# Kernel tuning notes

Hardware: AMD Instinct MI355X
Metric: run time of the kernel (lower is better)

Reference implementation:

```python
import jax, jax.numpy as jnp
import numpy as np
from jax import lax

B, L, D = 256, 512, 64
P, H, M, HOR, J = 256, 512, 256, 9, 12
EPS = 1e-5


def lstm_layer(xs, Wih, Whh, bih, bhh):
    """torch nn.LSTM single layer. xs: (B, L, Din). gates order i,f,g,o."""
    b, hdim = xs.shape[0], Whh.shape[1]
    WihT, WhhT = Wih.T, Whh.T
    bias = bih + bhh
    # precompute input contributions for all steps: (L, B, 4H)
    x_gates = jnp.swapaxes(xs @ WihT + bias, 0, 1)

    def step(carry, xg):
        h, c = carry
        gates = xg + h @ WhhT
        i, f, g, o = jnp.split(gates, 4, axis=-1)
        i = jax.nn.sigmoid(i)
        f = jax.nn.sigmoid(f)
        g = jnp.tanh(g)
        o = jax.nn.sigmoid(o)
        c = f * c + i * g
        h = o * jnp.tanh(c)
        return (h, c), h

    h0 = jnp.zeros((b, hdim), xs.dtype)
    c0 = jnp.zeros((b, hdim), xs.dtype)
    (_, _), hs = lax.scan(step, (h0, c0), x_gates)
    return jnp.swapaxes(hs, 0, 1)  # (B, L, H)


def setup_inputs() -> dict:
    key = jax.random.key(0)
    ks = jax.random.split(key, 16)
    g = lambda k, shape: (jax.random.normal(k, shape) * 0.05).astype(jnp.float32)
    z = lambda shape: jnp.zeros(shape, jnp.float32)
    return {
        "x": jax.random.normal(ks[0], (B, L, D), dtype=jnp.float32),
        "joint_index": jax.random.randint(ks[1], (B,), 0, J),
        "Wp": g(ks[2], (D, P)), "bp": z((P,)),
        "gamma": jnp.ones((P,), jnp.float32), "beta": z((P,)),
        "Wih0": g(ks[3], (4 * H, P)), "Whh0": g(ks[4], (4 * H, H)),
        "bih0": z((4 * H,)), "bhh0": z((4 * H,)),
        "Wih1": g(ks[5], (4 * H, H)), "Whh1": g(ks[6], (4 * H, H)),
        "bih1": z((4 * H,)), "bhh1": z((4 * H,)),
        "Wh1": g(ks[7], (J, H, M)), "bh1": z((J, M)),
        "Wh2": g(ks[8], (J, M, HOR)), "bh2": z((J, HOR)),
    }


def reference(x, joint_index, Wp, bp, gamma, beta,
              Wih0, Whh0, bih0, bhh0, Wih1, Whh1, bih1, bhh1,
              Wh1, bh1, Wh2, bh2):
    # input_proj: Linear -> LayerNorm -> GELU (exact erf form, torch default)
    h = x @ Wp + bp
    mu = h.mean(-1, keepdims=True)
    var = ((h - mu) ** 2).mean(-1, keepdims=True)
    h = gamma * (h - mu) * lax.rsqrt(var + EPS) + beta
    h = jax.nn.gelu(h, approximate=False)
    # 2-layer LSTM (dropout inactive at inference)
    h = lstm_layer(h, Wih0, Whh0, bih0, bhh0)
    h = lstm_layer(h, Wih1, Whh1, bih1, bhh1)
    h_last = h[:, -1, :]  # (B, H)
    # all 12 joint heads, then top-1 gather (matches torch stack+gather)
    z = jax.nn.gelu(jnp.einsum('bh,jhm->bjm', h_last, Wh1) + bh1, approximate=False)
    preds = jnp.einsum('bjm,jmo->bjo', z, Wh2) + bh2  # (B, J, HOR)
    return preds[jnp.arange(preds.shape[0]), joint_index]  # (B, HOR)
```

## Files before the change

kernel.cpp:

```cpp
#include <hip/hip_runtime.h>
#include <math.h>

typedef __bf16 bf16;
typedef __attribute__((ext_vector_type(8))) __bf16 bf16x8;
typedef __attribute__((ext_vector_type(4))) float f32x4;
typedef __attribute__((ext_vector_type(4))) int i32x4;

extern "C" __device__ i32x4 llvm_amdgcn_raw_buffer_load_v4i32(
    i32x4 rsrc, int voffset, int soffset, int cpol) __asm("llvm.amdgcn.raw.buffer.load.v4i32");

static constexpr int B = 256, L = 512, D = 64, P = 256, H = 512, M = 256, HOR = 9;
static constexpr int G = 2048;
static constexpr int K0 = P + H;
static constexpr int K1 = 2 * H;
static constexpr float EPS = 1e-5f;
static constexpr int NB = 6;
static constexpr int LDS_BYTES = 163840;

#define MFMA(a, b, c) __builtin_amdgcn_mfma_f32_16x16x32_bf16((a), (b), (c), 0, 0, 0)

__device__ __forceinline__ float sigmoidf_(float x) { return 1.0f / (1.0f + expf(-x)); }
__device__ __forceinline__ float gelu_exact(float x) {
    return 0.5f * x * (1.0f + erff(x * 0.70710678118654752f));
}

__device__ __forceinline__ void lds_barrier() {
    asm volatile("s_waitcnt lgkmcnt(0)" ::: "memory");
    __builtin_amdgcn_sched_barrier(0);
    __builtin_amdgcn_s_barrier();
    __builtin_amdgcn_sched_barrier(0);
}

__device__ __forceinline__ bf16x8 cload(const bf16* p) {
    union { unsigned long long u[2]; bf16x8 v; } r;
    const unsigned long long* q = (const unsigned long long*)p;
    r.u[0] = __hip_atomic_load(q,     __ATOMIC_RELAXED, __HIP_MEMORY_SCOPE_AGENT);
    r.u[1] = __hip_atomic_load(q + 1, __ATOMIC_RELAXED, __HIP_MEMORY_SCOPE_AGENT);
    return r.v;
}

__device__ __forceinline__ i32x4 make_rsrc(const void* p, unsigned bytes) {
    union { const void* p; unsigned u[2]; } a; a.p = p;
    i32x4 r;
    r.x = (int)a.u[0];
    r.y = (int)(a.u[1] & 0xFFFFu);
    r.z = (int)bytes;
    r.w = 0x00020000;
    return r;
}
__device__ __forceinline__ bf16x8 bload_sc0(i32x4 rsrc, int voff) {
    union { i32x4 i; bf16x8 b; } u;
    u.i = llvm_amdgcn_raw_buffer_load_v4i32(rsrc, voff, 0, 1 );
    return u.b;
}

__global__ __launch_bounds__(256) void emb_kernel(
    const float* __restrict__ x, const float* __restrict__ Wp,
    const float* __restrict__ bp, const float* __restrict__ gamma,
    const float* __restrict__ beta, bf16* __restrict__ ehi,
    bf16* __restrict__ elo, int use_elo)
{
    const int row = blockIdx.x;
    const int b   = row >> 9;
    const int t   = row & (L - 1);
    const int p   = threadIdx.x;
    __shared__ float xs[D];
    __shared__ float red[P];

    if (p < D) xs[p] = x[(size_t)row * D + p];
    __syncthreads();

    float acc = bp[p];
#pragma unroll
    for (int k = 0; k < D; ++k) acc = fmaf(xs[k], Wp[k * P + p], acc);

    red[p] = acc;
    __syncthreads();
    for (int s = 128; s > 0; s >>= 1) { if (p < s) red[p] += red[p + s]; __syncthreads(); }
    const float mu = red[0] * (1.0f / (float)P);
    __syncthreads();
    const float d = acc - mu;
    red[p] = d * d;
    __syncthreads();
    for (int s = 128; s > 0; s >>= 1) { if (p < s) red[p] += red[p + s]; __syncthreads(); }
    const float var = red[0] * (1.0f / (float)P);

    const float v = gelu_exact(gamma[p] * d * rsqrtf(var + EPS) + beta[p]);
    const size_t o = ((size_t)t * B + b) * P + p;
    const bf16 hh = (bf16)v;
    ehi[o] = hh;
    if (use_elo) elo[o] = (bf16)(v - (float)hh);
}

__global__ __launch_bounds__(64) void prep_w_frag(
    const float* __restrict__ Wih, const float* __restrict__ Whh, int Kih,
    bf16* __restrict__ hi, bf16* __restrict__ lo)
{
    const int ng = blockIdx.x, S = blockIdx.y, wc = blockIdx.z;
    const int lane = threadIdx.x;
    const int g = wc * 512 + ng * 16 + (lane & 15);
    const int kbase = S * 32 + (lane >> 4) * 8;
    const size_t out = ((((size_t)ng * gridDim.y + S) * 4 + wc) * 64 + lane) * 8;
#pragma unroll
    for (int e = 0; e < 8; ++e) {
        const int k = kbase + e;
        const float v = (k < Kih) ? Wih[(size_t)g * Kih + k]
                                  : Whh[(size_t)g * 512 + (k - Kih)];
        const bf16 h = (bf16)v;
        hi[out + e] = h;
        lo[out + e] = (bf16)(v - (float)h);
    }
}

__global__ __launch_bounds__(256) void prep_bias(
    const float* __restrict__ bih0, const float* __restrict__ bhh0,
    const float* __restrict__ bih1, const float* __restrict__ bhh1,
    float* __restrict__ bsum0, float* __restrict__ bsum1)
{
    const int g = blockIdx.x * 256 + threadIdx.x;
    bsum0[g] = bih0[g] + bhh0[g];
    bsum1[g] = bih1[g] + bhh1[g];
}

struct RArgs {
    int use_elo;
    const bf16 *ehi, *elo;
    const bf16 *W0hif, *W0lof, *W1hif, *W1lof;
    const float *bsum0, *bsum1;
    bf16 *h0hi[2], *h0lo[2], *h1hi[2], *h1lo[2];
    unsigned int* bar;
};

template <int NC, int LAYER>
__device__ __forceinline__ void tick_body(
    int tid, int lane, int wr2, int wc,
    int grow, int kin, int slot,
    const bf16* __restrict__ a0h, const bf16* __restrict__ a0l,
    i32x4 r1h, i32x4 r1l,
    char* lds, const bf16x8* wlo_own,
    float bI0, float bI1, float bF0, float bF1,
    float bG0, float bG1, float bO0, float bO1,
    float& c0r, float& c1r,
    unsigned int* hw_hi, unsigned int* hw_lo,
    int m, int jp)
{
    constexpr int K0seg = (LAYER == 0) ? 256 : 512;
    constexpr int AS0   = (LAYER == 0) ? 256 : 512;

    const bf16* wlds = (const bf16*)lds;
    char* dbuf = lds + 131072;
    float (*Gs)[68] = (float(*)[68])(lds + 131072);

    auto cloadA = [&](int c, int hf) -> bf16x8 {
        const int kk = c * 64 + kin;
        if (kk < K0seg) {
            const bf16* p = (hf ? a0l : a0h) + (size_t)grow * AS0 + kk;
            if (LAYER == 0) return *(const bf16x8*)p;
            return cload(p);
        }
        return bload_sc0(hf ? r1l : r1h, ((grow << 9) + (kk - K0seg)) * 2);
    };
    auto stageW = [&](const bf16x8& v, int pb, int hf) {
        *(bf16x8*)(dbuf + pb * 16384 + hf * 8192 + slot * 16) = v;
    };

    f32x4 hh[2], lh[2], hl[2];
#pragma unroll
    for (int i = 0; i < 2; ++i) {
        hh[i] = f32x4{0.f,0.f,0.f,0.f};
        lh[i] = f32x4{0.f,0.f,0.f,0.f};
        hl[i] = f32x4{0.f,0.f,0.f,0.f};
    }

    bf16x8 aregH[NB], aregL[NB];
#pragma unroll
    for (int i = 0; i < NB; ++i) { aregH[i] = cloadA(i, 0); aregL[i] = cloadA(i, 1); }
    stageW(aregH[0], 0, 0);
    stageW(aregL[0], 0, 1);
    aregH[0] = cloadA(NB, 0);
    aregL[0] = cloadA(NB, 1);
    lds_barrier();

#pragma unroll
    for (int c = 0; c < NC; ++c) {
        if (c + 1 < NC) {
            stageW(aregH[(c + 1) % NB], (c + 1) & 1, 0);
            stageW(aregL[(c + 1) % NB], (c + 1) & 1, 1);
            if (c + 1 + NB < NC) {
                aregH[(c + 1) % NB] = cloadA(c + 1 + NB, 0);
                aregL[(c + 1) % NB] = cloadA(c + 1 + NB, 1);
            }
        }
        const char* bufc = dbuf + (c & 1) * 16384;
#pragma unroll
        for (int s2 = 0; s2 < 2; ++s2) {
            const int S = c * 2 + s2;
            const int swz = ((s2 * 4) + (lane >> 4)) << 4;
            bf16x8 Whi = *(const bf16x8*)((const char*)wlds + ((S * 4 + wc) * 64 + lane) * 16);
            const bf16x8 Wlo = wlo_own[S];
#pragma unroll
            for (int rt = 0; rt < 2; ++rt) {
                const int row_tile = wr2 + rt * 2;
                const int ofsA = (((s2 * 4 + row_tile) * 64 + lane) * 16) ^ swz;
                bf16x8 Ahi = *(const bf16x8*)(bufc + ofsA);
                bf16x8 Alo = *(const bf16x8*)(bufc + 8192 + ofsA);
                hh[rt] = MFMA(Ahi, Whi, hh[rt]);
                lh[rt] = MFMA(Alo, Whi, lh[rt]);
                hl[rt] = MFMA(Ahi, Wlo, hl[rt]);
            }
        }
        lds_barrier();
    }

#pragma unroll
    for (int rt = 0; rt < 2; ++rt) {
        const int row_tile = wr2 + rt * 2;
#pragma unroll
        for (int r = 0; r < 4; ++r) {
            const int row = row_tile * 16 + (lane >> 4) * 4 + r;
            const int col = wc * 16 + (lane & 15);
            Gs[row][col] = hh[rt][r] + lh[rt][r] + hl[rt][r];
        }
    }
    lds_barrier();

    {
        float hv0, hv1;
        {
            const float iraw = Gs[m][jp]      + bI0;
            const float fraw = Gs[m][16 + jp] + bF0;
            const float graw = Gs[m][32 + jp] + bG0;
            const float oraw = Gs[m][48 + jp] + bO0;
            const float cv = sigmoidf_(fraw) * c0r + sigmoidf_(iraw) * tanhf(graw);
            c0r = cv;
            hv0 = sigmoidf_(oraw) * tanhf(cv);
        }
        {
            const float iraw = Gs[m][jp + 1]      + bI1;
            const float fraw = Gs[m][16 + jp + 1] + bF1;
            const float graw = Gs[m][32 + jp + 1] + bG1;
            const float oraw = Gs[m][48 + jp + 1] + bO1;
            const float cv = sigmoidf_(fraw) * c1r + sigmoidf_(iraw) * tanhf(graw);
            c1r = cv;
            hv1 = sigmoidf_(oraw) * tanhf(cv);
        }
        union { unsigned int u; bf16 b[2]; } ph, pl;
        ph.b[0] = (bf16)hv0; ph.b[1] = (bf16)hv1;
        pl.b[0] = (bf16)(hv0 - (float)ph.b[0]);
        pl.b[1] = (bf16)(hv1 - (float)ph.b[1]);
        __hip_atomic_store(hw_hi, ph.u, __ATOMIC_RELAXED, __HIP_MEMORY_SCOPE_AGENT);
        __hip_atomic_store(hw_lo, pl.u, __ATOMIC_RELAXED, __HIP_MEMORY_SCOPE_AGENT);
    }
}

__device__ __forceinline__ void group_bar(unsigned int* bar, int t) {
    __syncthreads();
    if (threadIdx.x == 0) {
        __hip_atomic_fetch_add(bar, 1u, __ATOMIC_RELAXED, __HIP_MEMORY_SCOPE_AGENT);
        const unsigned int target = 64u * (unsigned)(t + 1);
        while (__hip_atomic_load(bar, __ATOMIC_RELAXED, __HIP_MEMORY_SCOPE_AGENT) < target)
            __builtin_amdgcn_s_sleep(1);
        __builtin_amdgcn_fence(__ATOMIC_ACQUIRE, "workgroup");
    }
    __syncthreads();
}

__global__ __launch_bounds__(512, 1) void recurrence_kernel(RArgs a)
{
    extern __shared__ __align__(16) char lds[];

    const int bid   = blockIdx.x;
    const int layer = (bid >> 2) & 1;
    const int mg    = bid & 3;
    const int ng    = bid >> 3;
    const int bm0 = mg * 64, j0 = ng * 16;

    const int tid  = threadIdx.x;
    const int lane = tid & 63;
    const int wid  = tid >> 6;
    const int wr2 = wid >> 2, wc = wid & 3;

    const int row_s = tid >> 3;
    const int kq8   = tid & 7;
    const int s_loc = kq8 >> 2, k8 = kq8 & 3;
    const int slot  = (((s_loc * 4 + (row_s >> 4)) * 64) + k8 * 16 + (row_s & 15)) ^ kq8;
    const int grow  = bm0 + row_s;
    const int kin   = kq8 * 8;

    {
        const bf16* whif = layer ? a.W1hif : a.W0hif;
        const bf16* wsrc = whif + (size_t)ng * (size_t)(layer ? 65536 : 49152);
        const int NW = layer ? 16 : 12;
        for (int i = 0; i < NW; ++i) {
            const int ix = i * 512 + tid;
            ((bf16x8*)lds)[ix] = *(const bf16x8*)(wsrc + (size_t)ix * 8);
        }
    }
    __syncthreads();
    const bf16* wlo_blk = (layer ? a.W1lof : a.W0lof)
                          + (size_t)ng * (size_t)(layer ? 65536 : 49152);

    const int m  = (tid >> 3) & 63;
    const int jp = (tid & 7) * 2;
    const int j  = j0 + jp;
    const float* bs = layer ? a.bsum1 : a.bsum0;
    const float bI0 = bs[j],        bI1 = bs[j + 1];
    const float bF0 = bs[512 + j],  bF1 = bs[512 + j + 1];
    const float bG0 = bs[1024 + j], bG1 = bs[1024 + j + 1];
    const float bO0 = bs[1536 + j], bO1 = bs[1536 + j + 1];
    float c0r = 0.f, c1r = 0.f;
    const size_t hix = (size_t)(bm0 + m) * H + j;

    unsigned int* bar = a.bar + mg * 64;
    constexpr unsigned HB = (unsigned)(B * H * 2);

    if (layer == 0) {
        bf16x8 wlo_own[24];
#pragma unroll
        for (int S = 0; S < 24; ++S)
            wlo_own[S] = *(const bf16x8*)(wlo_blk + (size_t)((S * 4 + wc) * 64 + lane) * 8);

        for (int t = 0; t <= L; ++t) {
            const int p0 = t & 1;
            if (t < L) {
                const bf16* a0h = a.ehi + (size_t)t * B * P;
                const bf16* a0l = a.elo + (size_t)t * B * P;
                const i32x4 r1h = make_rsrc(a.h0hi[1 - p0], HB);
                const i32x4 r1l = make_rsrc(a.h0lo[1 - p0], HB);
                tick_body<12, 0>(tid, lane, wr2, wc, grow, kin, slot,
                                 a0h, a0l, r1h, r1l, lds, wlo_own,
                                 bI0, bI1, bF0, bF1, bG0, bG1, bO0, bO1,
                                 c0r, c1r,
                                 (unsigned int*)(a.h0hi[p0] + hix),
                                 (unsigned int*)(a.h0lo[p0] + hix), m, jp);
            }
            group_bar(bar, t);
        }
    } else {
        bf16x8 wlo_own[32];
#pragma unroll
        for (int S = 0; S < 32; ++S)
            wlo_own[S] = *(const bf16x8*)(wlo_blk + (size_t)((S * 4 + wc) * 64 + lane) * 8);

        for (int t = 0; t <= L; ++t) {
            const int p0 = t & 1;
            if (t >= 1) {
                const bf16* a0h = a.h0hi[1 - p0];
                const bf16* a0l = a.h0lo[1 - p0];
                const i32x4 r1h = make_rsrc(a.h1hi[p0], HB);
                const i32x4 r1l = make_rsrc(a.h1lo[p0], HB);
                tick_body<16, 1>(tid, lane, wr2, wc, grow, kin, slot,
                                 a0h, a0l, r1h, r1l, lds, wlo_own,
                                 bI0, bI1, bF0, bF1, bG0, bG1, bO0, bO1,
                                 c0r, c1r,
                                 (unsigned int*)(a.h1hi[1 - p0] + hix),
                                 (unsigned int*)(a.h1lo[1 - p0] + hix), m, jp);
            }
            group_bar(bar, t);
        }
    }
}

__global__ __launch_bounds__(256) void head_kernel(
    const bf16* __restrict__ h_hi, const bf16* __restrict__ h_lo,
    const int* __restrict__ joint_index,
    const float* __restrict__ Wh1, const float* __restrict__ bh1,
    const float* __restrict__ Wh2, const float* __restrict__ bh2,
    float* __restrict__ out)
{
    const int b = blockIdx.x;
    const int t = threadIdx.x;
    const int j = joint_index[b];
    __shared__ float hs[H];
    __shared__ float zs[M];

    hs[t]       = (float)h_hi[(size_t)b * H + t]       + (float)h_lo[(size_t)b * H + t];
    hs[t + 256] = (float)h_hi[(size_t)b * H + 256 + t] + (float)h_lo[(size_t)b * H + 256 + t];
    __syncthreads();

    float acc = bh1[j * M + t];
    const float* w = Wh1 + (size_t)j * H * M + t;
#pragma unroll 8
    for (int k = 0; k < H; ++k) acc = fmaf(hs[k], w[(size_t)k * M], acc);

    zs[t] = gelu_exact(acc);
    __syncthreads();

    if (t < HOR) {
        float a = bh2[j * HOR + t];
        const float* w2 = Wh2 + (size_t)j * M * HOR + t;
        for (int mm = 0; mm < M; ++mm) a = fmaf(zs[mm], w2[(size_t)mm * HOR], a);
        out[(size_t)b * HOR + t] = a;
    }
}

extern "C" void kernel_launch(void* const* d_in, const int* in_sizes, int n_in,
                              void* d_out, int out_size, void* d_ws, size_t ws_size,
                              hipStream_t stream)
{
    const float* x     = (const float*)d_in[0];
    const int*   joint = (const int*)  d_in[1];
    const float* Wp    = (const float*)d_in[2];
    const float* bp    = (const float*)d_in[3];
    const float* gamma = (const float*)d_in[4];
    const float* beta  = (const float*)d_in[5];
    const float* Wih0  = (const float*)d_in[6];
    const float* Whh0  = (const float*)d_in[7];
    const float* bih0  = (const float*)d_in[8];
    const float* bhh0  = (const float*)d_in[9];
    const float* Wih1  = (const float*)d_in[10];
    const float* Whh1  = (const float*)d_in[11];
    const float* bih1  = (const float*)d_in[12];
    const float* bhh1  = (const float*)d_in[13];
    const float* Wh1   = (const float*)d_in[14];
    const float* bh1   = (const float*)d_in[15];
    const float* Wh2   = (const float*)d_in[16];
    const float* bh2   = (const float*)d_in[17];
    float* out = (float*)d_out;

    char* base = (char*)d_ws;
    size_t off = 0;
    auto take = [&](size_t nbytes) -> void* {
        void* p = base + off;
        off = (off + nbytes + 255) & ~(size_t)255;
        return p;
    };

    RArgs a;
    a.W0hif = (bf16*)take((size_t)G * K0 * 2);
    a.W0lof = (bf16*)take((size_t)G * K0 * 2);
    a.W1hif = (bf16*)take((size_t)G * K1 * 2);
    a.W1lof = (bf16*)take((size_t)G * K1 * 2);
    a.bsum0 = (float*)take(G * 4);
    a.bsum1 = (float*)take(G * 4);

    const size_t states_off = off;
    for (int i = 0; i < 2; ++i) a.h0hi[i] = (bf16*)take((size_t)B * H * 2);
    for (int i = 0; i < 2; ++i) a.h0lo[i] = (bf16*)take((size_t)B * H * 2);
    for (int i = 0; i < 2; ++i) a.h1hi[i] = (bf16*)take((size_t)B * H * 2);
    for (int i = 0; i < 2; ++i) a.h1lo[i] = (bf16*)take((size_t)B * H * 2);
    a.bar = (unsigned int*)take(4 * 256);
    const size_t states_bytes = off - states_off;

    bf16* ehi = (bf16*)take((size_t)L * B * P * 2);
    bf16* elo = (bf16*)take((size_t)L * B * P * 2);
    a.use_elo = (off <= ws_size) ? 1 : 0;
    if (!a.use_elo) elo = ehi;
    a.ehi = ehi; a.elo = elo;

    prep_w_frag<<<dim3(32, K0 / 32, 4), 64, 0, stream>>>(Wih0, Whh0, P,
                                                         (bf16*)a.W0hif, (bf16*)a.W0lof);
    prep_w_frag<<<dim3(32, K1 / 32, 4), 64, 0, stream>>>(Wih1, Whh1, H,
                                                         (bf16*)a.W1hif, (bf16*)a.W1lof);
    prep_bias<<<8, 256, 0, stream>>>(bih0, bhh0, bih1, bhh1,
                                     (float*)a.bsum0, (float*)a.bsum1);
    hipMemsetAsync(base + states_off, 0, states_bytes, stream);
    emb_kernel<<<B * L, 256, 0, stream>>>(x, Wp, bp, gamma, beta, ehi, elo, a.use_elo);

    hipFuncSetAttribute((const void*)recurrence_kernel,
                        hipFuncAttributeMaxDynamicSharedMemorySize, LDS_BYTES);
    void* params[] = { &a };
    hipLaunchCooperativeKernel((void*)recurrence_kernel, dim3(256), dim3(512),
                               params, LDS_BYTES, stream);

    head_kernel<<<B, 256, 0, stream>>>(a.h1hi[1], a.h1lo[1], joint, Wh1, bh1, Wh2, bh2, out);
}
```

Measured before the change: 5.562 ms.

## Split K across wave pairs in LSTM recurrence tick with larger per-wave tiles

Changes the wave-to-tile mapping in the recurrence tick: each wave now computes a 2x2 block of 16x16 output tiles but only over alternating K chunks (split-K across wave pairs), reusing each loaded A fragment for two weight columns. Partial sums are combined through LDS with an extra barrier phase. This halves redundant A-fragment LDS reads per MFMA, but each wave idles on every other chunk while still waiting at every barrier, so per-wave MFMA work is unbalanced within each chunk. The global prefetch depth NB is also reduced from 6 to 4, likely to offset the extra accumulator registers.

```diff
diff --git a/kernel.cpp b/kernel.cpp
--- a/kernel.cpp
+++ b/kernel.cpp
@@ -14,7 +14,7 @@
 static constexpr int K0 = P + H;
 static constexpr int K1 = 2 * H;
 static constexpr float EPS = 1e-5f;
-static constexpr int NB = 6;
+static constexpr int NB = 4;
 static constexpr int LDS_BYTES = 163840;
 
 #define MFMA(a, b, c) __builtin_amdgcn_mfma_f32_16x16x32_bf16((a), (b), (c), 0, 0, 0)
@@ -133,7 +133,7 @@
 
 template <int NC, int LAYER>
 __device__ __forceinline__ void tick_body(
-    int tid, int lane, int wr2, int wc,
+    int tid, int lane, int rp, int cp, int kh,
     int grow, int kin, int slot,
     const bf16* __restrict__ a0h, const bf16* __restrict__ a0l,
     i32x4 r1h, i32x4 r1l,
@@ -164,13 +164,15 @@
         *(bf16x8*)(dbuf + pb * 16384 + hf * 8192 + slot * 16) = v;
     };
 
-    f32x4 hh[2], lh[2], hl[2];
-#pragma unroll
-    for (int i = 0; i < 2; ++i) {
-        hh[i] = f32x4{0.f,0.f,0.f,0.f};
-        lh[i] = f32x4{0.f,0.f,0.f,0.f};
-        hl[i] = f32x4{0.f,0.f,0.f,0.f};
-    }
+    f32x4 hh[2][2], lh[2][2], hl[2][2];
+#pragma unroll
+    for (int i = 0; i < 2; ++i)
+#pragma unroll
+        for (int k2 = 0; k2 < 2; ++k2) {
+            hh[i][k2] = f32x4{0.f,0.f,0.f,0.f};
+            lh[i][k2] = f32x4{0.f,0.f,0.f,0.f};
+            hl[i][k2] = f32x4{0.f,0.f,0.f,0.f};
+        }
 
     bf16x8 aregH[NB], aregL[NB];
 #pragma unroll
@@ -191,36 +193,59 @@
                 aregL[(c + 1) % NB] = cloadA(c + 1 + NB, 1);
             }
         }
-        const char* bufc = dbuf + (c & 1) * 16384;
-#pragma unroll
-        for (int s2 = 0; s2 < 2; ++s2) {
-            const int S = c * 2 + s2;
-            const int swz = ((s2 * 4) + (lane >> 4)) << 4;
-            bf16x8 Whi = *(const bf16x8*)((const char*)wlds + ((S * 4 + wc) * 64 + lane) * 16);
-            const bf16x8 Wlo = wlo_own[S];
-#pragma unroll
-            for (int rt = 0; rt < 2; ++rt) {
-                const int row_tile = wr2 + rt * 2;
-                const int ofsA = (((s2 * 4 + row_tile) * 64 + lane) * 16) ^ swz;
-                bf16x8 Ahi = *(const bf16x8*)(bufc + ofsA);
-                bf16x8 Alo = *(const bf16x8*)(bufc + 8192 + ofsA);
-                hh[rt] = MFMA(Ahi, Whi, hh[rt]);
-                lh[rt] = MFMA(Alo, Whi, lh[rt]);
-                hl[rt] = MFMA(Ahi, Wlo, hl[rt]);
+        if ((c & 1) == kh) {
+            const int cl = c >> 1;
+            const char* bufc = dbuf + (c & 1) * 16384;
+#pragma unroll
+            for (int s2 = 0; s2 < 2; ++s2) {
+                const int S = c * 2 + s2;
+                const int swz = ((s2 * 4) + (lane >> 4)) << 4;
+                bf16x8 Whi0 = *(const bf16x8*)((const char*)wlds + ((S * 4 + cp * 2    ) * 64 + lane) * 16);
+                bf16x8 Whi1 = *(const bf16x8*)((const char*)wlds + ((S * 4 + cp * 2 + 1) * 64 + lane) * 16);
+                const bf16x8 Wlo0 = wlo_own[(cl * 2 + s2) * 2 + 0];
+                const bf16x8 Wlo1 = wlo_own[(cl * 2 + s2) * 2 + 1];
+#pragma unroll
+                for (int rt = 0; rt < 2; ++rt) {
+                    const int row_tile = rp + rt * 2;
+                    const int ofsA = (((s2 * 4 + row_tile) * 64 + lane) * 16) ^ swz;
+                    bf16x8 Ahi = *(const bf16x8*)(bufc + ofsA);
+                    bf16x8 Alo = *(const bf16x8*)(bufc + 8192 + ofsA);
+                    hh[rt][0] = MFMA(Ahi, Whi0, hh[rt][0]);
+                    hh[rt][1] = MFMA(Ahi, Whi1, hh[rt][1]);
+                    lh[rt][0] = MFMA(Alo, Whi0, lh[rt][0]);
+                    lh[rt][1] = MFMA(Alo, Whi1, lh[rt][1]);
+                    hl[rt][0] = MFMA(Ahi, Wlo0, hl[rt][0]);
+                    hl[rt][1] = MFMA(Ahi, Wlo1, hl[rt][1]);
+                }
             }
         }
         lds_barrier();
     }
 
-#pragma unroll
-    for (int rt = 0; rt < 2; ++rt) {
-        const int row_tile = wr2 + rt * 2;
-#pragma unroll
-        for (int r = 0; r < 4; ++r) {
-            const int row = row_tile * 16 + (lane >> 4) * 4 + r;
-            const int col = wc * 16 + (lane & 15);
-            Gs[row][col] = hh[rt][r] + lh[rt][r] + hl[rt][r];
-        }
+    if (kh == 0) {
+#pragma unroll
+        for (int rt = 0; rt < 2; ++rt)
+#pragma unroll
+            for (int cc = 0; cc < 2; ++cc)
+#pragma unroll
+                for (int r = 0; r < 4; ++r) {
+                    const int row = (rp + rt * 2) * 16 + (lane >> 4) * 4 + r;
+                    const int col = (cp * 2 + cc) * 16 + (lane & 15);
+                    Gs[row][col] = hh[rt][cc][r] + lh[rt][cc][r] + hl[rt][cc][r];
+                }
+    }
+    lds_barrier();
+    if (kh == 1) {
+#pragma unroll
+        for (int rt = 0; rt < 2; ++rt)
+#pragma unroll
+            for (int cc = 0; cc < 2; ++cc)
+#pragma unroll
+                for (int r = 0; r < 4; ++r) {
+                    const int row = (rp + rt * 2) * 16 + (lane >> 4) * 4 + r;
+                    const int col = (cp * 2 + cc) * 16 + (lane & 15);
+                    Gs[row][col] += hh[rt][cc][r] + lh[rt][cc][r] + hl[rt][cc][r];
+                }
     }
     lds_barrier();
 
@@ -278,7 +303,9 @@
     const int tid  = threadIdx.x;
     const int lane = tid & 63;
     const int wid  = tid >> 6;
-    const int wr2 = wid >> 2, wc = wid & 3;
+    const int kh = wid & 1;
+    const int cp = (wid >> 1) & 1;
+    const int rp = wid >> 2;
 
     const int row_s = tid >> 3;
     const int kq8   = tid & 7;
@@ -317,8 +344,16 @@
     if (layer == 0) {
         bf16x8 wlo_own[24];
 #pragma unroll
-        for (int S = 0; S < 24; ++S)
-            wlo_own[S] = *(const bf16x8*)(wlo_blk + (size_t)((S * 4 + wc) * 64 + lane) * 8);
+        for (int cl = 0; cl < 6; ++cl)
+#pragma unroll
+            for (int s2 = 0; s2 < 2; ++s2)
+#pragma unroll
+                for (int cc = 0; cc < 2; ++cc) {
+                    const int S = (cl * 2 + kh) * 2 + s2;
+                    const int col = cp * 2 + cc;
+                    wlo_own[(cl * 2 + s2) * 2 + cc] =
+                        *(const bf16x8*)(wlo_blk + (size_t)((S * 4 + col) * 64 + lane) * 8);
+                }
 
         for (int t = 0; t <= L; ++t) {
             const int p0 = t & 1;
@@ -327,7 +362,7 @@
                 const bf16* a0l = a.elo + (size_t)t * B * P;
                 const i32x4 r1h = make_rsrc(a.h0hi[1 - p0], HB);
                 const i32x4 r1l = make_rsrc(a.h0lo[1 - p0], HB);
-                tick_body<12, 0>(tid, lane, wr2, wc, grow, kin, slot,
+                tick_body<12, 0>(tid, lane, rp, cp, kh, grow, kin, slot,
                                  a0h, a0l, r1h, r1l, lds, wlo_own,
                                  bI0, bI1, bF0, bF1, bG0, bG1, bO0, bO1,
                                  c0r, c1r,
@@ -339,8 +374,16 @@
     } else {
         bf16x8 wlo_own[32];
 #pragma unroll
-        for (int S = 0; S < 32; ++S)
-            wlo_own[S] = *(const bf16x8*)(wlo_blk + (size_t)((S * 4 + wc) * 64 + lane) * 8);
+        for (int cl = 0; cl < 8; ++cl)
+#pragma unroll
+            for (int s2 = 0; s2 < 2; ++s2)
+#pragma unroll
+                for (int cc = 0; cc < 2; ++cc) {
+                    const int S = (cl * 2 + kh) * 2 + s2;
+                    const int col = cp * 2 + cc;
+                    wlo_own[(cl * 2 + s2) * 2 + cc] =
+                        *(const bf16x8*)(wlo_blk + (size_t)((S * 4 + col) * 64 + lane) * 8);
+                }
 
         for (int t = 0; t <= L; ++t) {
             const int p0 = t & 1;
@@ -349,7 +392,7 @@
                 const bf16* a0l = a.h0lo[1 - p0];
                 const i32x4 r1h = make_rsrc(a.h1hi[p0], HB);
                 const i32x4 r1l = make_rsrc(a.h1lo[p0], HB);
-                tick_body<16, 1>(tid, lane, wr2, wc, grow, kin, slot,
+                tick_body<16, 1>(tid, lane, rp, cp, kh, grow, kin, slot,
                                  a0h, a0l, r1h, r1l, lds, wlo_own,
                                  bI0, bI1, bF0, bF1, bG0, bG1, bO0, bO1,
                                  c0r, c1r,
```

Result: slower. 7.207 ms (+29.6%).

## Switch recurrence GEMM to 32x32x16 MFMA with split-K across wave pairs

Applied to the files above, without the earlier changes.

Replaces the 16x16x32 MFMA tiling in the per-step LSTM gate GEMM with 32x32x16 MFMAs. Each wave now owns a 32x32 output tile and half of the K range, and the two K-halves are reduced through LDS in two phases with an extra barrier. The goal is fewer LDS operand reads and fewer MFMA issues per step. The extra barrier and LDS accumulation add latency on the serial recurrence path. The register prefetch depth NB also drops from 6 to 4, likely to offset the larger accumulators.

```diff
diff --git a/kernel.cpp b/kernel.cpp
--- a/kernel.cpp
+++ b/kernel.cpp
@@ -4,6 +4,7 @@
 typedef __bf16 bf16;
 typedef __attribute__((ext_vector_type(8))) __bf16 bf16x8;
 typedef __attribute__((ext_vector_type(4))) float f32x4;
+typedef __attribute__((ext_vector_type(16))) float f32x16;
 typedef __attribute__((ext_vector_type(4))) int i32x4;
 
 extern "C" __device__ i32x4 llvm_amdgcn_raw_buffer_load_v4i32(
@@ -14,10 +15,10 @@
 static constexpr int K0 = P + H;
 static constexpr int K1 = 2 * H;
 static constexpr float EPS = 1e-5f;
-static constexpr int NB = 6;
+static constexpr int NB = 4;
 static constexpr int LDS_BYTES = 163840;
 
-#define MFMA(a, b, c) __builtin_amdgcn_mfma_f32_16x16x32_bf16((a), (b), (c), 0, 0, 0)
+#define MFMA32(a, b, c) __builtin_amdgcn_mfma_f32_32x32x16_bf16((a), (b), (c), 0, 0, 0)
 
 __device__ __forceinline__ float sigmoidf_(float x) { return 1.0f / (1.0f + expf(-x)); }
 __device__ __forceinline__ float gelu_exact(float x) {
@@ -133,7 +134,7 @@
 
 template <int NC, int LAYER>
 __device__ __forceinline__ void tick_body(
-    int tid, int lane, int wr2, int wc,
+    int tid, int lane, int rp2, int cp2, int kh2,
     int grow, int kin, int slot,
     const bf16* __restrict__ a0h, const bf16* __restrict__ a0l,
     i32x4 r1h, i32x4 r1l,
@@ -151,6 +152,12 @@
     char* dbuf = lds + 131072;
     float (*Gs)[68] = (float(*)[68])(lds + 131072);
 
+    const int l15 = lane & 15;
+    const int lh4 = (lane >> 4) & 1;
+    const int l5  = lane >> 5;
+    const int rg  = rp2 * 2 + lh4;
+    const int wcw = cp2 * 2 + lh4;
+
     auto cloadA = [&](int c, int hf) -> bf16x8 {
         const int kk = c * 64 + kin;
         if (kk < K0seg) {
@@ -164,13 +171,9 @@
         *(bf16x8*)(dbuf + pb * 16384 + hf * 8192 + slot * 16) = v;
     };
 
-    f32x4 hh[2], lh[2], hl[2];
-#pragma unroll
-    for (int i = 0; i < 2; ++i) {
-        hh[i] = f32x4{0.f,0.f,0.f,0.f};
-        lh[i] = f32x4{0.f,0.f,0.f,0.f};
-        hl[i] = f32x4{0.f,0.f,0.f,0.f};
-    }
+    f32x16 hh, lh2, hl;
+#pragma unroll
+    for (int i = 0; i < 16; ++i) { hh[i] = 0.f; lh2[i] = 0.f; hl[i] = 0.f; }
 
     bf16x8 aregH[NB], aregL[NB];
 #pragma unroll
@@ -192,34 +195,39 @@
             }
         }
         const char* bufc = dbuf + (c & 1) * 16384;
-#pragma unroll
-        for (int s2 = 0; s2 < 2; ++s2) {
-            const int S = c * 2 + s2;
-            const int swz = ((s2 * 4) + (lane >> 4)) << 4;
-            bf16x8 Whi = *(const bf16x8*)((const char*)wlds + ((S * 4 + wc) * 64 + lane) * 16);
-            const bf16x8 Wlo = wlo_own[S];
-#pragma unroll
-            for (int rt = 0; rt < 2; ++rt) {
-                const int row_tile = wr2 + rt * 2;
-                const int ofsA = (((s2 * 4 + row_tile) * 64 + lane) * 16) ^ swz;
-                bf16x8 Ahi = *(const bf16x8*)(bufc + ofsA);
-                bf16x8 Alo = *(const bf16x8*)(bufc + 8192 + ofsA);
-                hh[rt] = MFMA(Ahi, Whi, hh[rt]);
-                lh[rt] = MFMA(Alo, Whi, lh[rt]);
-                hl[rt] = MFMA(Ahi, Wlo, hl[rt]);
-            }
+        const int Sg = c * 2 + kh2;
+#pragma unroll
+        for (int ks = 0; ks < 2; ++ks) {
+            const int q = ks * 2 + l5;
+            const int ofsA = (((kh2 * 4 + rg) * 64 + q * 16 + l15) * 16)
+                             ^ ((kh2 * 4 + q) << 4);
+            bf16x8 Ahi = *(const bf16x8*)(bufc + ofsA);
+            bf16x8 Alo = *(const bf16x8*)(bufc + 8192 + ofsA);
+            bf16x8 Whi = *(const bf16x8*)((const char*)wlds
+                           + ((Sg * 4 + wcw) * 64 + q * 16 + l15) * 16);
+            const bf16x8 Wlo = wlo_own[c * 2 + ks];
+            hh  = MFMA32(Ahi, Whi, hh);
+            lh2 = MFMA32(Alo, Whi, lh2);
+            hl  = MFMA32(Ahi, Wlo, hl);
         }
         lds_barrier();
     }
 
-#pragma unroll
-    for (int rt = 0; rt < 2; ++rt) {
-        const int row_tile = wr2 + rt * 2;
-#pragma unroll
-        for (int r = 0; r < 4; ++r) {
-            const int row = row_tile * 16 + (lane >> 4) * 4 + r;
-            const int col = wc * 16 + (lane & 15);
-            Gs[row][col] = hh[rt][r] + lh[rt][r] + hl[rt][r];
+    if (kh2 == 0) {
+#pragma unroll
+        for (int reg = 0; reg < 16; ++reg) {
+            const int row = rp2 * 32 + (reg & 3) + 8 * (reg >> 2) + 4 * l5;
+            const int col = cp2 * 32 + (lane & 31);
+            Gs[row][col] = hh[reg] + lh2[reg] + hl[reg];
+        }
+    }
+    lds_barrier();
+    if (kh2 == 1) {
+#pragma unroll
+        for (int reg = 0; reg < 16; ++reg) {
+            const int row = rp2 * 32 + (reg & 3) + 8 * (reg >> 2) + 4 * l5;
+            const int col = cp2 * 32 + (lane & 31);
+            Gs[row][col] += hh[reg] + lh2[reg] + hl[reg];
         }
     }
     lds_barrier();
@@ -278,7 +286,9 @@
     const int tid  = threadIdx.x;
     const int lane = tid & 63;
     const int wid  = tid >> 6;
-    const int wr2 = wid >> 2, wc = wid & 3;
+    const int kh2 = wid & 1;
+    const int cp2 = (wid >> 1) & 1;
+    const int rp2 = wid >> 2;
 
     const int row_s = tid >> 3;
     const int kq8   = tid & 7;
@@ -299,6 +309,9 @@
     __syncthreads();
     const bf16* wlo_blk = (layer ? a.W1lof : a.W0lof)
                           + (size_t)ng * (size_t)(layer ? 65536 : 49152);
+
+    const int l15 = lane & 15, lh4 = (lane >> 4) & 1, l5 = lane >> 5;
+    const int wcw = cp2 * 2 + lh4;
 
     const int m  = (tid >> 3) & 63;
     const int jp = (tid & 7) * 2;
@@ -317,8 +330,14 @@
     if (layer == 0) {
         bf16x8 wlo_own[24];
 #pragma unroll
-        for (int S = 0; S < 24; ++S)
-            wlo_own[S] = *(const bf16x8*)(wlo_blk + (size_t)((S * 4 + wc) * 64 + lane) * 8);
+        for (int cl = 0; cl < 12; ++cl)
+#pragma unroll
+            for (int ks = 0; ks < 2; ++ks) {
+                const int S = cl * 2 + kh2;
+                const int q = ks * 2 + l5;
+                wlo_own[cl * 2 + ks] = *(const bf16x8*)(
+                    wlo_blk + (size_t)((S * 4 + wcw) * 64 + q * 16 + l15) * 8);
+            }
 
         for (int t = 0; t <= L; ++t) {
             const int p0 = t & 1;
@@ -327,7 +346,7 @@
                 const bf16* a0l = a.elo + (size_t)t * B * P;
                 const i32x4 r1h = make_rsrc(a.h0hi[1 - p0], HB);
                 const i32x4 r1l = make_rsrc(a.h0lo[1 - p0], HB);
-                tick_body<12, 0>(tid, lane, wr2, wc, grow, kin, slot,
+                tick_body<12, 0>(tid, lane, rp2, cp2, kh2, grow, kin, slot,
                                  a0h, a0l, r1h, r1l, lds, wlo_own,
                                  bI0, bI1, bF0, bF1, bG0, bG1, bO0, bO1,
                                  c0r, c1r,
@@ -339,8 +358,14 @@
     } else {
         bf16x8 wlo_own[32];
 #pragma unroll
-        for (int S = 0; S < 32; ++S)
-            wlo_own[S] = *(const bf16x8*)(wlo_blk + (size_t)((S * 4 + wc) * 64 + lane) * 8);
+        for (int cl = 0; cl < 16; ++cl)
+#pragma unroll
+            for (int ks = 0; ks < 2; ++ks) {
+                const int S = cl * 2 + kh2;
+                const int q = ks * 2 + l5;
+                wlo_own[cl * 2 + ks] = *(const bf16x8*)(
+                    wlo_blk + (size_t)((S * 4 + wcw) * 64 + q * 16 + l15) * 8);
+            }
 
         for (int t = 0; t <= L; ++t) {
             const int p0 = t & 1;
@@ -349,7 +374,7 @@
                 const bf16* a0l = a.h0lo[1 - p0];
                 const i32x4 r1h = make_rsrc(a.h1hi[p0], HB);
                 const i32x4 r1l = make_rsrc(a.h1lo[p0], HB);
-                tick_body<16, 1>(tid, lane, wr2, wc, grow, kin, slot,
+                tick_body<16, 1>(tid, lane, rp2, cp2, kh2, grow, kin, slot,
                                  a0h, a0l, r1h, r1l, lds, wlo_own,
                                  bI0, bI1, bF0, bF1, bG0, bG1, bO0, bO1,
                                  c0r, c1r,
```

Result: slower. 6.016 ms (+8.2%).
